# Kernel optimization log

Hardware: AMD Instinct MI355X
Metric: run time of the kernel (lower is better)

The kernel has to match this reference:

```python
import jax, jax.numpy as jnp
import numpy as np

B, N1, N2, C1, C2 = 8, 8192, 2048, 128, 256
O1, O2 = 256, 256
IN_CH = C2 + C1  # 384
BN_EPS = 1e-5


def setup_inputs() -> dict:
    key = jax.random.key(0)
    ks = jax.random.split(key, 6)
    return {
        "xyz1": jax.random.normal(ks[0], (B, N1, 3), dtype=jnp.float32),
        "xyz2": jax.random.normal(ks[1], (B, N2, 3), dtype=jnp.float32),
        "feats1": jax.random.normal(ks[2], (B, C1, N1), dtype=jnp.float32),
        "feats2": jax.random.normal(ks[3], (B, C2, N2), dtype=jnp.float32),
        "W1": jax.random.normal(ks[4], (O1, IN_CH), dtype=jnp.float32) * 0.02,
        "b1": jnp.zeros((O1,), jnp.float32),
        "g1": jnp.ones((O1,), jnp.float32),
        "be1": jnp.zeros((O1,), jnp.float32),
        "W2": jax.random.normal(ks[5], (O2, O1), dtype=jnp.float32) * 0.02,
        "b2": jnp.zeros((O2,), jnp.float32),
        "g2": jnp.ones((O2,), jnp.float32),
        "be2": jnp.zeros((O2,), jnp.float32),
    }


def _bn(x, g, b):
    # eval-mode BatchNorm1d with init running stats (mean=0, var=1)
    return g[None, :, None] * x * (1.0 / jnp.sqrt(1.0 + BN_EPS)) + b[None, :, None]


def reference(xyz1, xyz2, feats1, feats2, W1, b1, g1, be1, W2, b2, g2, be2):
    # pairwise Euclidean distances (B, N1, N2), torch.cdist equivalent
    d2 = (jnp.sum(xyz1 * xyz1, -1)[:, :, None]
          + jnp.sum(xyz2 * xyz2, -1)[:, None, :]
          - 2.0 * jnp.einsum('bnc,bmc->bnm', xyz1, xyz2))
    d = jnp.sqrt(jnp.maximum(d2, 0.0))
    # 3 nearest neighbors (smallest distances)
    neg_d, idx = jax.lax.top_k(-d, 3)          # idx: (B, N1, 3)
    knn_d = jnp.maximum(-neg_d, 1e-8)
    w = 1.0 / knn_d
    w = w / jnp.sum(w, -1, keepdims=True)       # (B, N1, 3)
    # gather neighbor features: feats2 (B,C2,N2) -> (B,N2,C2) -> (B,N1,3,C2)
    f2p = jnp.swapaxes(feats2, 1, 2)
    neigh = f2p[jnp.arange(B)[:, None, None], idx]
    out = jnp.einsum('bnk,bnkc->bcn', w, neigh)  # (B, C2, N1)
    out = jnp.concatenate([out, feats1], axis=1)  # (B, C2+C1, N1)
    # Conv1d(k=1) + BN + ReLU, twice
    h = jax.nn.relu(_bn(jnp.einsum('oc,bcn->bon', W1, out) + b1[None, :, None], g1, be1))
    h = jax.nn.relu(_bn(jnp.einsum('oc,bcn->bon', W2, h) + b2[None, :, None], g2, be2))
    return h
```

## Files before the change

### kernel.cpp

```cpp
#include <hip/hip_runtime.h>

typedef __attribute__((ext_vector_type(8))) short bf16x8;
typedef __attribute__((ext_vector_type(4))) float f32x4;
typedef __attribute__((ext_vector_type(4))) unsigned short u16x4;

__device__ __forceinline__ unsigned short f2bf(float f) {
  unsigned u = __float_as_uint(f);
  u += 0x7FFFu + ((u >> 16) & 1u);
  return (unsigned short)(u >> 16);
}

__global__ __launch_bounds__(256) void prep(
    const float* __restrict__ f1, const float* __restrict__ f2,
    const float* __restrict__ xyz2,
    const float* __restrict__ W1, const float* __restrict__ W2,
    short* __restrict__ ft1, unsigned short* __restrict__ ft2,
    short* __restrict__ wpk1, short* __restrict__ wpk2,
    float4* __restrict__ xyz2s) {
  __shared__ float tile[64][65];
  const int bid = blockIdx.x, t = threadIdx.x;
  if (bid < 1024) {
    int b = bid & 7, i = bid >> 3;
    int j0 = (i & 31) * 64, c0 = (i >> 5) * 64;
    int r = t >> 4, c4 = (t & 15) * 4;
#pragma unroll
    for (int p = 0; p < 4; ++p) {
      int ci = p * 16 + r;
      float4 v = *(const float4*)&f2[(size_t)(b * 256 + c0 + ci) * 2048 + j0 + c4];
      tile[ci][c4] = v.x; tile[ci][c4 + 1] = v.y;
      tile[ci][c4 + 2] = v.z; tile[ci][c4 + 3] = v.w;
    }
    __syncthreads();
#pragma unroll
    for (int p = 0; p < 4; ++p) {
      int jr = p * 16 + r;
      u16x4 o;
#pragma unroll
      for (int k = 0; k < 4; ++k) o[k] = f2bf(tile[c4 + k][jr]);
      *(u16x4*)&ft2[(size_t)(b * 2048 + j0 + jr) * 256 + c0 + c4] = o;
    }
  } else if (bid < 3072) {
    int i = bid - 1024;
    int b = i & 7, ii = i >> 3;
    int j0 = (ii & 127) * 64, c0 = (ii >> 7) * 64;
    int r = t >> 4, c4 = (t & 15) * 4;
#pragma unroll
    for (int p = 0; p < 4; ++p) {
      int ci = p * 16 + r;
      float4 v = *(const float4*)&f1[(size_t)(b * 128 + c0 + ci) * 8192 + j0 + c4];
      tile[ci][c4] = v.x; tile[ci][c4 + 1] = v.y;
      tile[ci][c4 + 2] = v.z; tile[ci][c4 + 3] = v.w;
    }
    __syncthreads();
#pragma unroll
    for (int p = 0; p < 4; ++p) {
      int jr = p * 16 + r;
      u16x4 o;
#pragma unroll
      for (int k = 0; k < 4; ++k) o[k] = f2bf(tile[c4 + k][jr]);
      *(u16x4*)&ft1[((size_t)b * 8192 + j0 + jr) * 128 + c0 + c4] = o;
    }
  } else {
    int id = (bid - 3072) * 256 + t;
    if (id < 98304) {
      int j = id & 7, lane = (id >> 3) & 63, mt = (id >> 9) & 15, kt = id >> 13;
      int o = mt * 16 + (lane & 15);
      int c = kt * 32 + ((lane >> 4) & 3) * 8 + j;
      wpk1[id] = (short)f2bf(W1[o * 384 + c]);
    } else if (id < 163840) {
      int f = id - 98304;
      int j = f & 7, lane = (f >> 3) & 63, mt = (f >> 9) & 15, kt = f >> 13;
      int o = mt * 16 + (lane & 15);
      int c = kt * 32 + ((lane >> 4) & 3) * 8 + j;
      wpk2[f] = (short)f2bf(W2[o * 256 + c]);
    } else {
      int p = id - 163840;
      int b = p >> 11, j = p & 2047;
      const float* q = xyz2 + (size_t)(b * 2048 + j) * 3;
      float px = q[0], py = q[1], pz = q[2];
      float s2 = __fadd_rn(__fadd_rn(__fmul_rn(px, px), __fmul_rn(py, py)),
                           __fmul_rn(pz, pz));
      xyz2s[b * 2048 + j] = make_float4(px, py, pz, s2);
    }
  }
}

__device__ __forceinline__ void merge44d(double a0, double a1, double a2, double a3,
                                         double c0, double c1, double c2, double c3,
                                         double& o0, double& o1, double& o2, double& o3) {
#define POP(OD)                                                           \
  {                                                                       \
    bool s = a0 < c0;                                                     \
    OD = s ? a0 : c0;                                                     \
    double sa0 = s ? a1 : a0, sa1 = s ? a2 : a1, sa2 = s ? a3 : a2;       \
    double sc0 = s ? c0 : c1, sc1 = s ? c1 : c2, sc2 = s ? c2 : c3;       \
    a3 = s ? 1e300 : a3; c3 = s ? c3 : 1e300;                             \
    a0 = sa0; a1 = sa1; a2 = sa2; c0 = sc0; c1 = sc1; c2 = sc2;           \
  }
  POP(o0) POP(o1) POP(o2) POP(o3)
#undef POP
}

__global__ __launch_bounds__(512) void fused(
    const float* __restrict__ xyz1, const float4* __restrict__ xyz2s,
    const unsigned short* __restrict__ ft2, const short* __restrict__ ft1,
    const short* __restrict__ wpk1, const short* __restrict__ wpk2,
    const float* __restrict__ b1, const float* __restrict__ g1, const float* __restrict__ be1,
    const float* __restrict__ b2, const float* __restrict__ g2, const float* __restrict__ be2,
    float* __restrict__ out) {
  __shared__ __align__(16) char XH[32768];
  __shared__ __align__(16) double T4[1024];
  float* W3s = (float*)((char*)T4 + 6144);
  int*  ID3s = (int*)((char*)T4 + 6912);

  const int t = threadIdx.x, lane = t & 63, wid = t >> 6;
  const int blk = blockIdx.x;
  const int b = blk & 7, n0 = (blk >> 3) * 64;
  const int l15 = lane & 15, l4 = lane >> 4;

  {
    float4* pkB = (float4*)XH;
    for (int j = t; j < 2048; j += 512) pkB[j] = xyz2s[b * 2048 + j];
  }
  float qx, qy, qz, s1;
  {
    const float* p = xyz1 + ((size_t)b * 8192 + n0 + lane) * 3;
    qx = p[0]; qy = p[1]; qz = p[2];
    s1 = __fadd_rn(__fadd_rn(__fmul_rn(qx, qx), __fmul_rn(qy, qy)), __fmul_rn(qz, qz));
  }
  __syncthreads();

  unsigned k0 = 0xFFFFFFFFu, k1 = 0xFFFFFFFFu, k2 = 0xFFFFFFFFu, k3 = 0xFFFFFFFFu;
  unsigned i0 = 0, i1 = 0, i2 = 0, i3 = 0;
  {
    const float4* __restrict__ pkB = (const float4*)XH;
    const int jb = wid * 256;
#pragma unroll 4
    for (int jo = 0; jo < 256; ++jo) {
      int j = jb + jo;
      float4 P = pkB[j];
      float dot = __fadd_rn(__fadd_rn(__fmul_rn(qx, P.x), __fmul_rn(qy, P.y)),
                            __fmul_rn(qz, P.z));
      float d2 = __fsub_rn(__fadd_rn(s1, P.w), __fadd_rn(dot, dot));
      unsigned K = __float_as_uint(fmaxf(d2, 0.0f));
      bool l0 = K < k0, l1 = K < k1, l2 = K < k2, l3 = K < k3;
      unsigned nk0 = min(k0, K);
      unsigned nk1 = min(max(K, k0), k1);
      unsigned nk2 = min(max(K, k1), k2);
      unsigned nk3 = min(max(K, k2), k3);
      unsigned uj = (unsigned)j;
      unsigned ni0 = l0 ? uj : i0;
      unsigned ni1 = l0 ? i0 : (l1 ? uj : i1);
      unsigned ni2 = l1 ? i1 : (l2 ? uj : i2);
      unsigned ni3 = l2 ? i2 : (l3 ? uj : i3);
      k0 = nk0; k1 = nk1; k2 = nk2; k3 = nk3;
      i0 = ni0; i1 = ni1; i2 = ni2; i3 = ni3;
    }
  }
  double key0 = fma((double)k0, 2048.0, (double)i0);
  double key1 = fma((double)k1, 2048.0, (double)i1);
  double key2 = fma((double)k2, 2048.0, (double)i2);
  double key3 = fma((double)k3, 2048.0, (double)i3);

  if (wid >= 4) {
    int w = wid - 4;
    T4[0 * 256 + w * 64 + lane] = key0; T4[1 * 256 + w * 64 + lane] = key1;
    T4[2 * 256 + w * 64 + lane] = key2; T4[3 * 256 + w * 64 + lane] = key3;
  }
  __syncthreads();
  double m10 = 0, m11 = 0, m12 = 0, m13 = 0;
  if (wid < 4) {
    double p0 = T4[0 * 256 + wid * 64 + lane], p1 = T4[1 * 256 + wid * 64 + lane];
    double p2 = T4[2 * 256 + wid * 64 + lane], p3 = T4[3 * 256 + wid * 64 + lane];
    merge44d(key0, key1, key2, key3, p0, p1, p2, p3, m10, m11, m12, m13);
  }
  __syncthreads();
  if (wid == 2 || wid == 3) {
    int w = wid - 2;
    T4[0 * 128 + w * 64 + lane] = m10; T4[1 * 128 + w * 64 + lane] = m11;
    T4[2 * 128 + w * 64 + lane] = m12; T4[3 * 128 + w * 64 + lane] = m13;
  }
  __syncthreads();
  double m20 = 0, m21 = 0, m22 = 0, m23 = 0;
  if (wid < 2) {
    double p0 = T4[0 * 128 + wid * 64 + lane], p1 = T4[1 * 128 + wid * 64 + lane];
    double p2 = T4[2 * 128 + wid * 64 + lane], p3 = T4[3 * 128 + wid * 64 + lane];
    merge44d(m10, m11, m12, m13, p0, p1, p2, p3, m20, m21, m22, m23);
  }
  __syncthreads();
  if (wid == 1) {
    T4[0 * 64 + lane] = m20; T4[1 * 64 + lane] = m21;
    T4[2 * 64 + lane] = m22; T4[3 * 64 + lane] = m23;
  }
  __syncthreads();
  if (wid == 0) {
    double p0 = T4[0 * 64 + lane], p1 = T4[1 * 64 + lane];
    double p2 = T4[2 * 64 + lane], p3 = T4[3 * 64 + lane];
    double mf[4];
    merge44d(m20, m21, m22, m23, p0, p1, p2, p3, mf[0], mf[1], mf[2], mf[3]);
    float e[4]; int ji[4];
#pragma unroll
    for (int s = 0; s < 4; ++s) {
      double qd = mf[s] * (1.0 / 2048.0);
      double qf = trunc(qd);
      double jd = fma(-qf, 2048.0, mf[s]);
      ji[s] = (int)jd;
      e[s] = __fsqrt_rn(__uint_as_float((unsigned)qf));
    }
#define SW(X, Y)                                                          \
  {                                                                       \
    bool sw = (e[X] > e[Y]) || ((e[X] == e[Y]) && (ji[X] > ji[Y]));       \
    float td = e[X]; int ti = ji[X];                                      \
    e[X] = sw ? e[Y] : e[X]; ji[X] = sw ? ji[Y] : ji[X];                  \
    e[Y] = sw ? td : e[Y];   ji[Y] = sw ? ti : ji[Y];                     \
  }
    SW(0, 1) SW(1, 2) SW(2, 3) SW(0, 1) SW(1, 2) SW(0, 1)
#undef SW
    float c0 = fmaxf(e[0], 1e-8f), c1 = fmaxf(e[1], 1e-8f), c2 = fmaxf(e[2], 1e-8f);
    float u0 = 1.0f / c0, u1 = 1.0f / c1, u2 = 1.0f / c2;
    float ss = __fadd_rn(__fadd_rn(u0, u1), u2);
    W3s[lane * 3 + 0] = u0 / ss; W3s[lane * 3 + 1] = u1 / ss; W3s[lane * 3 + 2] = u2 / ss;
    ID3s[lane * 3 + 0] = ji[0]; ID3s[lane * 3 + 1] = ji[1]; ID3s[lane * 3 + 2] = ji[2];
  }
  __syncthreads();

  {
    const int c = t & 255, half = t >> 8;
    const size_t f2b = (size_t)b * 2048 * 256;
#pragma unroll 2
    for (int qi = 0; qi < 32; ++qi) {
      int q = half * 32 + qi;
      int j0 = ID3s[q * 3 + 0], j1 = ID3s[q * 3 + 1], j2 = ID3s[q * 3 + 2];
      float W0 = W3s[q * 3 + 0], W1v = W3s[q * 3 + 1], W2v = W3s[q * 3 + 2];
      float v0 = __uint_as_float((unsigned)ft2[f2b + (size_t)j0 * 256 + c] << 16);
      float v1 = __uint_as_float((unsigned)ft2[f2b + (size_t)j1 * 256 + c] << 16);
      float v2 = __uint_as_float((unsigned)ft2[f2b + (size_t)j2 * 256 + c] << 16);
      float v = W0 * v0 + W1v * v1 + W2v * v2;
      int addr = (q * 512 + c * 2) ^ ((q & 7) << 4);
      *(unsigned short*)(XH + addr) = f2bf(v);
    }
  }
  __syncthreads();

  f32x4 acc[2][4];
#pragma unroll
  for (int m = 0; m < 2; ++m)
#pragma unroll
    for (int n = 0; n < 4; ++n) acc[m][n] = (f32x4){0.f, 0.f, 0.f, 0.f};

#pragma unroll
  for (int kt = 0; kt < 8; ++kt) {
    bf16x8 a[2], bb[4];
#pragma unroll
    for (int m = 0; m < 2; ++m)
      a[m] = *(const bf16x8*)(wpk1 + ((size_t)(kt * 16 + wid * 2 + m) * 64 + lane) * 8);
#pragma unroll
    for (int nt = 0; nt < 4; ++nt) {
      int q = nt * 16 + l15;
      int addr = q * 512 + ((kt * 64 + l4 * 16) ^ ((q & 7) << 4));
      bb[nt] = *(const bf16x8*)(XH + addr);
    }
#pragma unroll
    for (int m = 0; m < 2; ++m)
#pragma unroll
      for (int nt = 0; nt < 4; ++nt)
        acc[m][nt] = __builtin_amdgcn_mfma_f32_16x16x32_bf16(a[m], bb[nt], acc[m][nt], 0, 0, 0);
  }
#pragma unroll
  for (int kt = 8; kt < 12; ++kt) {
    bf16x8 a[2], bb[4];
#pragma unroll
    for (int m = 0; m < 2; ++m)
      a[m] = *(const bf16x8*)(wpk1 + ((size_t)(kt * 16 + wid * 2 + m) * 64 + lane) * 8);
#pragma unroll
    for (int nt = 0; nt < 4; ++nt)
      bb[nt] = *(const bf16x8*)(ft1 + ((size_t)b * 8192 + n0 + nt * 16 + l15) * 128 +
                                (kt - 8) * 32 + l4 * 8);
#pragma unroll
    for (int m = 0; m < 2; ++m)
#pragma unroll
      for (int nt = 0; nt < 4; ++nt)
        acc[m][nt] = __builtin_amdgcn_mfma_f32_16x16x32_bf16(a[m], bb[nt], acc[m][nt], 0, 0, 0);
  }
  __syncthreads();

  const float BNINV = 0.99999500003749972f;
#pragma unroll
  for (int m = 0; m < 2; ++m) {
    int cb = wid * 32 + m * 16 + l4 * 4;
    float gv[4], bv[4], ev[4];
#pragma unroll
    for (int r = 0; r < 4; ++r) {
      gv[r] = g1[cb + r] * BNINV; bv[r] = b1[cb + r]; ev[r] = be1[cb + r];
    }
#pragma unroll
    for (int nt = 0; nt < 4; ++nt) {
      int q = nt * 16 + l15;
      u16x4 pk4;
#pragma unroll
      for (int r = 0; r < 4; ++r)
        pk4[r] = f2bf(fmaxf((acc[m][nt][r] + bv[r]) * gv[r] + ev[r], 0.0f));
      *(u16x4*)(XH + ((q * 512 + cb * 2) ^ ((q & 7) << 4))) = pk4;
    }
  }
  __syncthreads();

#pragma unroll
  for (int m = 0; m < 2; ++m)
#pragma unroll
    for (int n = 0; n < 4; ++n) acc[m][n] = (f32x4){0.f, 0.f, 0.f, 0.f};
#pragma unroll
  for (int kt = 0; kt < 8; ++kt) {
    bf16x8 a[2], bb[4];
#pragma unroll
    for (int m = 0; m < 2; ++m)
      a[m] = *(const bf16x8*)(wpk2 + ((size_t)(kt * 16 + wid * 2 + m) * 64 + lane) * 8);
#pragma unroll
    for (int nt = 0; nt < 4; ++nt) {
      int q = nt * 16 + l15;
      int addr = q * 512 + ((kt * 64 + l4 * 16) ^ ((q & 7) << 4));
      bb[nt] = *(const bf16x8*)(XH + addr);
    }
#pragma unroll
    for (int m = 0; m < 2; ++m)
#pragma unroll
      for (int nt = 0; nt < 4; ++nt)
        acc[m][nt] = __builtin_amdgcn_mfma_f32_16x16x32_bf16(a[m], bb[nt], acc[m][nt], 0, 0, 0);
  }

#pragma unroll
  for (int m = 0; m < 2; ++m) {
    int ob = wid * 32 + m * 16 + l4 * 4;
    float gv[4], bv[4], ev[4];
#pragma unroll
    for (int r = 0; r < 4; ++r) {
      gv[r] = g2[ob + r] * BNINV; bv[r] = b2[ob + r]; ev[r] = be2[ob + r];
    }
#pragma unroll
    for (int nt = 0; nt < 4; ++nt) {
      int nn = n0 + nt * 16 + l15;
#pragma unroll
      for (int r = 0; r < 4; ++r)
        out[((size_t)b * 256 + ob + r) * 8192 + nn] =
            fmaxf((acc[m][nt][r] + bv[r]) * gv[r] + ev[r], 0.0f);
    }
  }
}

extern "C" void kernel_launch(void* const* d_in, const int* in_sizes, int n_in,
                              void* d_out, int out_size, void* d_ws, size_t ws_size,
                              hipStream_t stream) {
  (void)in_sizes; (void)n_in; (void)out_size; (void)ws_size;
  const float* xyz1   = (const float*)d_in[0];
  const float* xyz2   = (const float*)d_in[1];
  const float* feats1 = (const float*)d_in[2];
  const float* feats2 = (const float*)d_in[3];
  const float* W1  = (const float*)d_in[4];
  const float* b1  = (const float*)d_in[5];
  const float* g1  = (const float*)d_in[6];
  const float* be1 = (const float*)d_in[7];
  const float* W2  = (const float*)d_in[8];
  const float* b2  = (const float*)d_in[9];
  const float* g2  = (const float*)d_in[10];
  const float* be2 = (const float*)d_in[11];
  float* out = (float*)d_out;

  char* ws = (char*)d_ws;
  short*          wpk1  = (short*)(ws);
  short*          wpk2  = (short*)(ws + 196608);
  float4*         xyz2s = (float4*)(ws + 327680);
  unsigned short* ft2   = (unsigned short*)(ws + 589824);
  short*          ft1   = (short*)(ws + 8978432);

  prep<<<3776, 256, 0, stream>>>(feats1, feats2, xyz2, W1, W2,
                                 ft1, ft2, wpk1, wpk2, xyz2s);
  fused<<<1024, 512, 0, stream>>>(xyz1, xyz2s, ft2, ft1, wpk1, wpk2,
                                  b1, g1, be1, b2, g2, be2, out);
}
```

Before: 249.7 us.

## Pack index into distance key low bits and use med3 top-8 selection

Replaces the separate key/index top-4 insertion with a single 32-bit key whose low 11 mantissa bits hold the neighbor index. An 8-deep sorted list is kept with v_med3_u32, and the cross-wave double-precision merges become unsigned bitonic merges. Exact distances for the 8 candidates are then recomputed and sorted to recover the exact top-3. xyz2 is now read directly from global memory instead of being staged in LDS. This removes per-step compare/select work on the indices and the double-precision arithmetic. The cost is extra global loads, plus reliance on 8 truncated-key candidates being enough to contain the true top-3.

```diff
diff --git a/kernel.cpp b/kernel.cpp
--- a/kernel.cpp
+++ b/kernel.cpp
@@ -8,6 +8,12 @@
   unsigned u = __float_as_uint(f);
   u += 0x7FFFu + ((u >> 16) & 1u);
   return (unsigned short)(u >> 16);
+}
+
+__device__ __forceinline__ unsigned med3u(unsigned a, unsigned b, unsigned c) {
+  unsigned r;
+  asm("v_med3_u32 %0, %1, %2, %3" : "=v"(r) : "v"(a), "v"(b), "v"(c));
+  return r;
 }
 
 __global__ __launch_bounds__(256) void prep(
@@ -85,20 +91,20 @@
   }
 }
 
-__device__ __forceinline__ void merge44d(double a0, double a1, double a2, double a3,
-                                         double c0, double c1, double c2, double c3,
-                                         double& o0, double& o1, double& o2, double& o3) {
-#define POP(OD)                                                           \
-  {                                                                       \
-    bool s = a0 < c0;                                                     \
-    OD = s ? a0 : c0;                                                     \
-    double sa0 = s ? a1 : a0, sa1 = s ? a2 : a1, sa2 = s ? a3 : a2;       \
-    double sc0 = s ? c0 : c1, sc1 = s ? c1 : c2, sc2 = s ? c2 : c3;       \
-    a3 = s ? 1e300 : a3; c3 = s ? c3 : 1e300;                             \
-    a0 = sa0; a1 = sa1; a2 = sa2; c0 = sc0; c1 = sc1; c2 = sc2;           \
-  }
-  POP(o0) POP(o1) POP(o2) POP(o3)
-#undef POP
+__device__ __forceinline__ void ceu(unsigned& x, unsigned& y) {
+  unsigned lo = min(x, y), hi = max(x, y);
+  x = lo; y = hi;
+}
+__device__ __forceinline__ void merge8(unsigned k[8], const unsigned p[8]) {
+  unsigned m0 = min(k[0], p[7]), m1 = min(k[1], p[6]);
+  unsigned m2 = min(k[2], p[5]), m3 = min(k[3], p[4]);
+  unsigned m4 = min(k[4], p[3]), m5 = min(k[5], p[2]);
+  unsigned m6 = min(k[6], p[1]), m7 = min(k[7], p[0]);
+  ceu(m0, m4); ceu(m1, m5); ceu(m2, m6); ceu(m3, m7);
+  ceu(m0, m2); ceu(m1, m3); ceu(m4, m6); ceu(m5, m7);
+  ceu(m0, m1); ceu(m2, m3); ceu(m4, m5); ceu(m6, m7);
+  k[0] = m0; k[1] = m1; k[2] = m2; k[3] = m3;
+  k[4] = m4; k[5] = m5; k[6] = m6; k[7] = m7;
 }
 
 __global__ __launch_bounds__(512) void fused(
@@ -109,103 +115,119 @@
     const float* __restrict__ b2, const float* __restrict__ g2, const float* __restrict__ be2,
     float* __restrict__ out) {
   __shared__ __align__(16) char XH[32768];
-  __shared__ __align__(16) double T4[1024];
-  float* W3s = (float*)((char*)T4 + 6144);
-  int*  ID3s = (int*)((char*)T4 + 6912);
+  __shared__ float W3s[192];
+  __shared__ int   ID3s[192];
+  unsigned* MG = (unsigned*)XH;
 
   const int t = threadIdx.x, lane = t & 63, wid = t >> 6;
   const int blk = blockIdx.x;
   const int b = blk & 7, n0 = (blk >> 3) * 64;
   const int l15 = lane & 15, l4 = lane >> 4;
 
-  {
-    float4* pkB = (float4*)XH;
-    for (int j = t; j < 2048; j += 512) pkB[j] = xyz2s[b * 2048 + j];
-  }
   float qx, qy, qz, s1;
   {
     const float* p = xyz1 + ((size_t)b * 8192 + n0 + lane) * 3;
     qx = p[0]; qy = p[1]; qz = p[2];
     s1 = __fadd_rn(__fadd_rn(__fmul_rn(qx, qx), __fmul_rn(qy, qy)), __fmul_rn(qz, qz));
   }
-  __syncthreads();
-
-  unsigned k0 = 0xFFFFFFFFu, k1 = 0xFFFFFFFFu, k2 = 0xFFFFFFFFu, k3 = 0xFFFFFFFFu;
-  unsigned i0 = 0, i1 = 0, i2 = 0, i3 = 0;
+
+  unsigned k[8];
+#pragma unroll
+  for (int s = 0; s < 8; ++s) k[s] = 0xFFFFFFFFu;
   {
-    const float4* __restrict__ pkB = (const float4*)XH;
-    const int jb = wid * 256;
+    const float4* __restrict__ pk = xyz2s + (size_t)b * 2048;
+    const int jb = __builtin_amdgcn_readfirstlane(wid * 256);
 #pragma unroll 4
     for (int jo = 0; jo < 256; ++jo) {
       int j = jb + jo;
-      float4 P = pkB[j];
+      float4 P = pk[j];
       float dot = __fadd_rn(__fadd_rn(__fmul_rn(qx, P.x), __fmul_rn(qy, P.y)),
                             __fmul_rn(qz, P.z));
       float d2 = __fsub_rn(__fadd_rn(s1, P.w), __fadd_rn(dot, dot));
-      unsigned K = __float_as_uint(fmaxf(d2, 0.0f));
-      bool l0 = K < k0, l1 = K < k1, l2 = K < k2, l3 = K < k3;
-      unsigned nk0 = min(k0, K);
-      unsigned nk1 = min(max(K, k0), k1);
-      unsigned nk2 = min(max(K, k1), k2);
-      unsigned nk3 = min(max(K, k2), k3);
-      unsigned uj = (unsigned)j;
-      unsigned ni0 = l0 ? uj : i0;
-      unsigned ni1 = l0 ? i0 : (l1 ? uj : i1);
-      unsigned ni2 = l1 ? i1 : (l2 ? uj : i2);
-      unsigned ni3 = l2 ? i2 : (l3 ? uj : i3);
-      k0 = nk0; k1 = nk1; k2 = nk2; k3 = nk3;
-      i0 = ni0; i1 = ni1; i2 = ni2; i3 = ni3;
-    }
-  }
-  double key0 = fma((double)k0, 2048.0, (double)i0);
-  double key1 = fma((double)k1, 2048.0, (double)i1);
-  double key2 = fma((double)k2, 2048.0, (double)i2);
-  double key3 = fma((double)k3, 2048.0, (double)i3);
+      unsigned K = (__float_as_uint(fmaxf(d2, 0.0f)) & 0xFFFFF800u) | (unsigned)j;
+      unsigned nk0 = min(k[0], K);
+      unsigned nk1 = med3u(K, k[0], k[1]);
+      unsigned nk2 = med3u(K, k[1], k[2]);
+      unsigned nk3 = med3u(K, k[2], k[3]);
+      unsigned nk4 = med3u(K, k[3], k[4]);
+      unsigned nk5 = med3u(K, k[4], k[5]);
+      unsigned nk6 = med3u(K, k[5], k[6]);
+      unsigned nk7 = med3u(K, k[6], k[7]);
+      k[0] = nk0; k[1] = nk1; k[2] = nk2; k[3] = nk3;
+      k[4] = nk4; k[5] = nk5; k[6] = nk6; k[7] = nk7;
+    }
+  }
 
   if (wid >= 4) {
-    int w = wid - 4;
-    T4[0 * 256 + w * 64 + lane] = key0; T4[1 * 256 + w * 64 + lane] = key1;
-    T4[2 * 256 + w * 64 + lane] = key2; T4[3 * 256 + w * 64 + lane] = key3;
-  }
-  __syncthreads();
-  double m10 = 0, m11 = 0, m12 = 0, m13 = 0;
+    int wl = (wid - 4) * 64 + lane;
+#pragma unroll
+    for (int s = 0; s < 8; ++s) MG[s * 256 + wl] = k[s];
+  }
+  __syncthreads();
   if (wid < 4) {
-    double p0 = T4[0 * 256 + wid * 64 + lane], p1 = T4[1 * 256 + wid * 64 + lane];
-    double p2 = T4[2 * 256 + wid * 64 + lane], p3 = T4[3 * 256 + wid * 64 + lane];
-    merge44d(key0, key1, key2, key3, p0, p1, p2, p3, m10, m11, m12, m13);
+    unsigned p[8];
+    int wl = wid * 64 + lane;
+#pragma unroll
+    for (int s = 0; s < 8; ++s) p[s] = MG[s * 256 + wl];
+    merge8(k, p);
   }
   __syncthreads();
   if (wid == 2 || wid == 3) {
-    int w = wid - 2;
-    T4[0 * 128 + w * 64 + lane] = m10; T4[1 * 128 + w * 64 + lane] = m11;
-    T4[2 * 128 + w * 64 + lane] = m12; T4[3 * 128 + w * 64 + lane] = m13;
-  }
-  __syncthreads();
-  double m20 = 0, m21 = 0, m22 = 0, m23 = 0;
+    int wl = (wid - 2) * 64 + lane;
+#pragma unroll
+    for (int s = 0; s < 8; ++s) MG[s * 128 + wl] = k[s];
+  }
+  __syncthreads();
   if (wid < 2) {
-    double p0 = T4[0 * 128 + wid * 64 + lane], p1 = T4[1 * 128 + wid * 64 + lane];
-    double p2 = T4[2 * 128 + wid * 64 + lane], p3 = T4[3 * 128 + wid * 64 + lane];
-    merge44d(m10, m11, m12, m13, p0, p1, p2, p3, m20, m21, m22, m23);
+    unsigned p[8];
+    int wl = wid * 64 + lane;
+#pragma unroll
+    for (int s = 0; s < 8; ++s) p[s] = MG[s * 128 + wl];
+    merge8(k, p);
   }
   __syncthreads();
   if (wid == 1) {
-    T4[0 * 64 + lane] = m20; T4[1 * 64 + lane] = m21;
-    T4[2 * 64 + lane] = m22; T4[3 * 64 + lane] = m23;
+#pragma unroll
+    for (int s = 0; s < 8; ++s) MG[s * 64 + lane] = k[s];
   }
   __syncthreads();
   if (wid == 0) {
-    double p0 = T4[0 * 64 + lane], p1 = T4[1 * 64 + lane];
-    double p2 = T4[2 * 64 + lane], p3 = T4[3 * 64 + lane];
-    double mf[4];
-    merge44d(m20, m21, m22, m23, p0, p1, p2, p3, mf[0], mf[1], mf[2], mf[3]);
+    unsigned p[8];
+#pragma unroll
+    for (int s = 0; s < 8; ++s) p[s] = MG[s * 64 + lane];
+    merge8(k, p);
+
+    unsigned db[8], jj[8];
+    const float4* __restrict__ pk = xyz2s + (size_t)b * 2048;
+#pragma unroll
+    for (int s = 0; s < 8; ++s) {
+      unsigned j = k[s] & 2047u;
+      float4 P = pk[j];
+      float dot = __fadd_rn(__fadd_rn(__fmul_rn(qx, P.x), __fmul_rn(qy, P.y)),
+                            __fmul_rn(qz, P.z));
+      float d2 = __fsub_rn(__fadd_rn(s1, P.w), __fadd_rn(dot, dot));
+      db[s] = __float_as_uint(fmaxf(d2, 0.0f));
+      jj[s] = j;
+    }
+#define CEP(X, Y)                                                         \
+  {                                                                       \
+    bool s_ = (db[X] < db[Y]) || ((db[X] == db[Y]) && (jj[X] < jj[Y]));   \
+    unsigned td_ = db[X], ti_ = jj[X];                                    \
+    db[X] = s_ ? db[X] : db[Y]; jj[X] = s_ ? jj[X] : jj[Y];               \
+    db[Y] = s_ ? db[Y] : td_;   jj[Y] = s_ ? jj[Y] : ti_;                 \
+  }
+    CEP(0, 1) CEP(2, 3) CEP(4, 5) CEP(6, 7)
+    CEP(0, 2) CEP(1, 3) CEP(4, 6) CEP(5, 7)
+    CEP(1, 2) CEP(5, 6)
+    CEP(0, 4) CEP(1, 5) CEP(2, 6) CEP(3, 7)
+    CEP(2, 4) CEP(3, 5)
+    CEP(1, 2) CEP(3, 4) CEP(5, 6)
+#undef CEP
     float e[4]; int ji[4];
 #pragma unroll
     for (int s = 0; s < 4; ++s) {
-      double qd = mf[s] * (1.0 / 2048.0);
-      double qf = trunc(qd);
-      double jd = fma(-qf, 2048.0, mf[s]);
-      ji[s] = (int)jd;
-      e[s] = __fsqrt_rn(__uint_as_float((unsigned)qf));
+      e[s] = __fsqrt_rn(__uint_as_float(db[s]));
+      ji[s] = (int)jj[s];
     }
 #define SW(X, Y)                                                          \
   {                                                                       \
```

Result: faster. 230.1 us (-7.8%).
